# Kernel tuning notes

Hardware: AMD Instinct MI355X
Metric: run time of the kernel (lower is better)

The kernel has to match this reference:

```python
import jax, jax.numpy as jnp
import numpy as np

NEG = -1e4      # BigBird additive mask value
LN_EPS = 1e-12  # BERT-style LayerNorm eps


def _bigbird_forward(xs_pad, mask, Wq, bq, Wk, bk, Wv, bv, Wo, bo, gamma, beta, rand_idx):
    b, n, hsz = xs_pad.shape
    H = rand_idx.shape[0]
    nb = rand_idx.shape[1] + 2          # one rand row per non-edge query block
    BS = n // nb                        # block size
    d = hsz // H
    r = rand_idx.shape[2]
    scale = 1.0 / np.sqrt(d).astype(np.float32)

    mf = mask.reshape(b, n).astype(xs_pad.dtype)   # (b,n) 1=token, 0=pad
    mb = mf.reshape(b, nb, BS)                     # blocked mask

    def proj(W, bias):
        return (xs_pad @ W + bias).reshape(b, n, H, d).transpose(0, 2, 1, 3)

    q = proj(Wq, bq) * scale            # (b,H,n,d)
    k = proj(Wk, bk)
    v = proj(Wv, bv)
    qb = q.reshape(b, H, nb, BS, d)
    kb = k.reshape(b, H, nb, BS, d)
    vb = v.reshape(b, H, nb, BS, d)

    # ---- global rows: first / last query block attend to all keys ----
    def full_row(qi):                   # qi: (b,H,BS,d)
        s = jnp.einsum('bhqd,bhkd->bhqk', qi, k) + (1.0 - mf)[:, None, None, :] * NEG
        return jnp.einsum('bhqk,bhkd->bhqd', jax.nn.softmax(s, axis=-1), v)

    ctx_first = full_row(qb[:, :, 0])
    ctx_last = full_row(qb[:, :, nb - 1])

    # ---- random key/value blocks: per-head, per-query-block gather ----
    hidx = jnp.arange(H)[:, None, None]
    rand_k = kb[:, hidx, rand_idx].reshape(b, H, nb - 2, r * BS, d)
    rand_v = vb[:, hidx, rand_idx].reshape(b, H, nb - 2, r * BS, d)
    rand_m = mb[:, rand_idx].reshape(b, H, nb - 2, r * BS)

    def sparse_row(qi, kc, vc, mc):     # kc:(b,H,K,d), mc:(b,H,K)
        s = jnp.einsum('bhqd,bhkd->bhqk', qi, kc) + (1.0 - mc)[:, :, None, :] * NEG
        return jnp.einsum('bhqk,bhkd->bhqd', jax.nn.softmax(s, axis=-1), vc)

    def gather_blocks(ids, ridx):
        kc = jnp.concatenate([kb[:, :, j] for j in ids] + [rand_k[:, :, ridx]], axis=2)
        vc = jnp.concatenate([vb[:, :, j] for j in ids] + [rand_v[:, :, ridx]], axis=2)
        mc = jnp.concatenate([jnp.broadcast_to(mb[:, None, j], (b, H, BS)) for j in ids]
                             + [rand_m[:, :, ridx]], axis=2)
        return kc, vc, mc

    # second / penultimate query blocks: window + globals + rand
    ctx_second = sparse_row(qb[:, :, 1], *gather_blocks([0, 1, 2, nb - 1], 0))
    ctx_penult = sparse_row(qb[:, :, nb - 2], *gather_blocks([nb - 3, nb - 2, nb - 1, 0], nb - 3))

    # ---- middle rows i in [2, nb-3]: 3-block sliding window + first/last global + r random ----
    nmid = nb - 4
    mid = jnp.arange(2, nb - 2)
    win = mid[:, None] + jnp.arange(-1, 2)[None, :]        # (nmid,3)
    k_win = kb[:, :, win].reshape(b, H, nmid, 3 * BS, d)
    v_win = vb[:, :, win].reshape(b, H, nmid, 3 * BS, d)
    m_win = jnp.broadcast_to(mb[:, win].reshape(b, 1, nmid, 3 * BS), (b, H, nmid, 3 * BS))

    def rep_glob(t):                     # (b,H,BS,...) -> (b,H,nmid,BS,...)
        return jnp.broadcast_to(t[:, :, None], (b, H, nmid) + t.shape[2:])

    k_mid = jnp.concatenate([k_win, rep_glob(kb[:, :, 0]), rep_glob(kb[:, :, nb - 1]),
                             rand_k[:, :, 1:nb - 3]], axis=3)
    v_mid = jnp.concatenate([v_win, rep_glob(vb[:, :, 0]), rep_glob(vb[:, :, nb - 1]),
                             rand_v[:, :, 1:nb - 3]], axis=3)
    m_first = jnp.broadcast_to(mb[:, None, None, 0], (b, H, nmid, BS))
    m_last = jnp.broadcast_to(mb[:, None, None, nb - 1], (b, H, nmid, BS))
    m_mid = jnp.concatenate([m_win, m_first, m_last, rand_m[:, :, 1:nb - 3]], axis=3)

    s_mid = jnp.einsum('bhmqd,bhmkd->bhmqk', qb[:, :, 2:nb - 2], k_mid) \
            + (1.0 - m_mid)[:, :, :, None, :] * NEG
    ctx_mid = jnp.einsum('bhmqk,bhmkd->bhmqd', jax.nn.softmax(s_mid, axis=-1), v_mid)

    ctx = jnp.concatenate([ctx_first[:, :, None], ctx_second[:, :, None], ctx_mid,
                           ctx_penult[:, :, None], ctx_last[:, :, None]], axis=2)
    ctx = ctx.reshape(b, H, n, d).transpose(0, 2, 1, 3).reshape(b, n, hsz)
    ctx = ctx * mf[:, :, None]           # from_mask on output rows

    # BigBirdSelfOutput: dense + residual + LayerNorm (dropout=0 / eval)
    y = ctx @ Wo + bo + xs_pad
    mu = y.mean(-1, keepdims=True)
    var = ((y - mu) ** 2).mean(-1, keepdims=True)
    return (y - mu) * jax.lax.rsqrt(var + LN_EPS) * gamma + beta


def setup_inputs() -> dict:
    key = jax.random.key(0)
    ks = jax.random.split(key, 6)
    B, N, HSZ, H, BS, R = 4, 4096, 1024, 16, 64, 3
    NB = N // BS
    init = lambda k, shp: jax.random.normal(k, shp, dtype=jnp.float32) * 0.02
    return {
        'xs_pad': jax.random.normal(ks[0], (B, N, HSZ), dtype=jnp.float32),
        'mask': jnp.ones((B, 1, N), dtype=jnp.int32),
        'Wq': init(ks[1], (HSZ, HSZ)), 'bq': jnp.zeros((HSZ,), jnp.float32),
        'Wk': init(ks[2], (HSZ, HSZ)), 'bk': jnp.zeros((HSZ,), jnp.float32),
        'Wv': init(ks[3], (HSZ, HSZ)), 'bv': jnp.zeros((HSZ,), jnp.float32),
        'Wo': init(ks[4], (HSZ, HSZ)), 'bo': jnp.zeros((HSZ,), jnp.float32),
        'gamma': jnp.ones((HSZ,), jnp.float32), 'beta': jnp.zeros((HSZ,), jnp.float32),
        'rand_idx': jax.random.randint(ks[5], (H, NB - 2, R), 1, NB - 1).astype(jnp.int32),
    }


def reference(xs_pad, mask, Wq, bq, Wk, bk, Wv, bv, Wo, bo, gamma, beta, rand_idx):
    return _bigbird_forward(xs_pad, mask, Wq, bq, Wk, bk, Wv, bv, Wo, bo, gamma, beta, rand_idx)
```

## Files before the change

### kernel.cpp

```cpp
#include <hip/hip_runtime.h>
#include <hip/hip_bf16.h>

#define B_   4
#define N_   4096
#define HSZ  1024
#define H_   16
#define D_   64
#define NB_  64
#define R_   3
#define M_   (B_*N_)
#define NEGV (-1e4f)
#define LOG2E 1.4426950408889634f

typedef float f32x4 __attribute__((ext_vector_type(4)));
typedef short s16x8 __attribute__((ext_vector_type(8)));
typedef __bf16 b16x8 __attribute__((ext_vector_type(8)));

__device__ __forceinline__ f32x4 mfma16(s16x8 a, s16x8 b, f32x4 c) {
  return __builtin_amdgcn_mfma_f32_16x16x32_bf16(
      __builtin_bit_cast(b16x8, a), __builtin_bit_cast(b16x8, b), c, 0, 0, 0);
}

__device__ __forceinline__ short f2b(float x) {
  __hip_bfloat16 h = __float2bfloat16(x);
  return (short)__builtin_bit_cast(unsigned short, h);
}

__device__ __forceinline__ unsigned pack2(float a, float b) {
  return (unsigned)(unsigned short)f2b(a) |
         ((unsigned)(unsigned short)f2b(b) << 16);
}

__device__ __forceinline__ void gl_lds16(const short* g, short* l) {
  __builtin_amdgcn_global_load_lds(
      (const __attribute__((address_space(1))) unsigned int*)g,
      (__attribute__((address_space(3))) unsigned int*)l, 16, 0, 0);
}

__global__ __launch_bounds__(256) void k_conv(const float* __restrict__ in,
                                              short* __restrict__ out) {
  size_t i = ((size_t)blockIdx.x * 256 + threadIdx.x) * 8;
  float4 a = *(const float4*)&in[i];
  float4 b = *(const float4*)&in[i + 4];
  s16x8 o;
  o[0] = f2b(a.x); o[1] = f2b(a.y); o[2] = f2b(a.z); o[3] = f2b(a.w);
  o[4] = f2b(b.x); o[5] = f2b(b.y); o[6] = f2b(b.z); o[7] = f2b(b.w);
  *(s16x8*)&out[i] = o;
}

__global__ __launch_bounds__(256) void k_wt(const float* __restrict__ Wq,
                                            const float* __restrict__ Wk,
                                            const float* __restrict__ Wv,
                                            const float* __restrict__ Wo,
                                            short* __restrict__ out) {
  const int z = blockIdx.z;
  const float* src = (z == 0) ? Wq : (z == 1) ? Wk : (z == 2) ? Wv : Wo;
  short* dst = out + (size_t)z * HSZ * HSZ;
  __shared__ __align__(16) float t[64][68];
  const int tk = blockIdx.x * 64, tn = blockIdx.y * 64;
  const int tid = threadIdx.x;
#pragma unroll
  for (int r = 0; r < 4; ++r) {
    int c = tid + r * 256;
    int row = c >> 4, seg = c & 15;
    *(float4*)&t[row][seg * 4] =
        *(const float4*)&src[(size_t)(tk + row) * HSZ + tn + seg * 4];
  }
  __syncthreads();
#pragma unroll
  for (int r = 0; r < 2; ++r) {
    int c = tid + r * 256;
    int row = c >> 3, seg = c & 7;
    s16x8 o;
#pragma unroll
    for (int u = 0; u < 8; ++u) o[u] = f2b(t[seg * 8 + u][row]);
    *(s16x8*)&dst[(size_t)(tn + row) * HSZ + tk + seg * 8] = o;
  }
}

template <int PATH>
__global__ __launch_bounds__(256) void k_gemm(
    const short* __restrict__ A, const short* __restrict__ WT,
    const float* __restrict__ bias0, const float* __restrict__ bias1,
    short* __restrict__ o0, short* __restrict__ o1,
    const float* __restrict__ xs, float* __restrict__ yout) {
  const int z = (PATH == 0) ? blockIdx.z : 0;
  const int wsel = (PATH == 0) ? z : (PATH == 1 ? 2 : 3);
  const short* Bt = WT + (size_t)wsel * HSZ * HSZ;
  const float* bias = (PATH == 0 && z == 1) ? bias1 : bias0;
  short* outb = (PATH == 0 && z == 1) ? o1 : o0;
  const float alpha = (PATH == 0 && z == 0) ? 0.125f * LOG2E : 1.0f;

  __shared__ __align__(16) short a_lds[2][128][64];
  __shared__ __align__(16) short b_lds[2][128][64];

  const int tid = threadIdx.x, lane = tid & 63, wave = tid >> 6;
  const int lq = lane & 15, g = lane >> 4;
  const int wm = (wave & 1) * 64, wn = (wave >> 1) * 64;
  const int tm = blockIdx.x * 128, tn = blockIdx.y * 128;

  const int srow = wave * 32 + (lane >> 3);
  const int scol = ((lane & 7) ^ ((lane >> 3) & 7)) * 8;

  f32x4 acc[4][4] = {};

  auto STAGE = [&](int buf, int kt) {
#pragma unroll
    for (int u = 0; u < 4; ++u) {
      gl_lds16(&A[(size_t)(tm + srow + u * 8) * HSZ + kt + scol],
               &a_lds[buf][wave * 32 + u * 8][0]);
      gl_lds16(&Bt[(size_t)(tn + srow + u * 8) * HSZ + kt + scol],
               &b_lds[buf][wave * 32 + u * 8][0]);
    }
  };

  const int sw = (lq & 7) << 3;
  auto COMPUTE = [&](int buf) {
#pragma unroll
    for (int kk = 0; kk < 2; ++kk) {
      const int ko = (kk * 32 + g * 8) ^ sw;
      s16x8 af[4], bf[4];
#pragma unroll
      for (int i = 0; i < 4; ++i)
        af[i] = *(const s16x8*)&a_lds[buf][wm + i * 16 + lq][ko];
#pragma unroll
      for (int j = 0; j < 4; ++j)
        bf[j] = *(const s16x8*)&b_lds[buf][wn + j * 16 + lq][ko];
#pragma unroll
      for (int i = 0; i < 4; ++i)
#pragma unroll
        for (int j = 0; j < 4; ++j)
          acc[i][j] = (PATH == 1) ? mfma16(af[i], bf[j], acc[i][j])
                                  : mfma16(bf[j], af[i], acc[i][j]);
    }
  };

  STAGE(0, 0);
  STAGE(1, 64);
  int cur = 0;
  for (int s = 0; s < 14; ++s) {
    asm volatile("s_waitcnt vmcnt(8)" ::: "memory");
    __builtin_amdgcn_s_barrier();
    COMPUTE(cur);
    __builtin_amdgcn_s_barrier();
    STAGE(cur, (s + 2) * 64);
    cur ^= 1;
  }
  asm volatile("s_waitcnt vmcnt(8)" ::: "memory");
  __builtin_amdgcn_s_barrier();
  COMPUTE(cur);
  cur ^= 1;
  asm volatile("s_waitcnt vmcnt(0)" ::: "memory");
  __builtin_amdgcn_s_barrier();
  COMPUTE(cur);

  if (PATH == 1) {
#pragma unroll
    for (int j = 0; j < 4; ++j) {
      const int col = tn + wn + j * 16 + lq;
      const int hh = col >> 6, dd = col & 63;
      const float bi = bias[col];
#pragma unroll
      for (int i = 0; i < 4; ++i) {
        const int nrow = tm + wm + i * 16 + g * 4;
        const int bb = nrow >> 12, nn = nrow & (N_ - 1);
        uint2 w;
        w.x = pack2(acc[i][j][0] + bi, acc[i][j][1] + bi);
        w.y = pack2(acc[i][j][2] + bi, acc[i][j][3] + bi);
        *(uint2*)&o0[(((size_t)bb * H_ + hh) * D_ + dd) * N_ + nn] = w;
      }
    }
    return;
  }

#pragma unroll
  for (int i = 0; i < 4; ++i) {
    const int row = tm + wm + i * 16 + lq;
#pragma unroll
    for (int j = 0; j < 4; ++j) {
      const int colb = tn + wn + j * 16 + g * 4;
      const float4 bi = *(const float4*)&bias[colb];
      if (PATH == 0) {
        const int bb = row >> 12, nn = row & (N_ - 1);
        const int hh = colb >> 6, dd = colb & 63;
        uint2 w;
        w.x = pack2((acc[i][j][0] + bi.x) * alpha,
                    (acc[i][j][1] + bi.y) * alpha);
        w.y = pack2((acc[i][j][2] + bi.z) * alpha,
                    (acc[i][j][3] + bi.w) * alpha);
        *(uint2*)&outb[(((size_t)bb * H_ + hh) * N_ + nn) * D_ + dd] = w;
      } else {
        const size_t idx = (size_t)row * HSZ + colb;
        const float4 xv = *(const float4*)&xs[idx];
        float4 yv;
        yv.x = acc[i][j][0] + bi.x + xv.x;
        yv.y = acc[i][j][1] + bi.y + xv.y;
        yv.z = acc[i][j][2] + bi.z + xv.z;
        yv.w = acc[i][j][3] + bi.w + xv.w;
        *(float4*)&yout[idx] = yv;
      }
    }
  }
}

__global__ __launch_bounds__(256) void k_attn(
    const short* __restrict__ Q, const short* __restrict__ K,
    const short* __restrict__ VT, const int* __restrict__ mask,
    const int* __restrict__ rnd, short* __restrict__ ctx,
    float* __restrict__ pO, float* __restrict__ pm, float* __restrict__ pl) {
  const int orig = blockIdx.x;
  const int swg = (orig & 7) * 624 + (orig >> 3);
  const int s = swg % 78;
  const int bh_i = swg / 78;
  const int h = bh_i & 15, b = bh_i >> 4;
  const int tid = threadIdx.x, lane = tid & 63, wave = tid >> 6;
  const int g = lane >> 4, lq = lane & 15;

  __shared__ __align__(16) short k_lds[64][64];
  __shared__ __align__(16) short vt_lds[64][64];
  __shared__ __align__(16) short p_lds[4][16][72];
  __shared__ __align__(16) float bias_s[64];
  __shared__ int list_s[8];
  __shared__ int Ls;

  const bool mid = (s < 62);
  const int qb = mid ? (s + 1) : (((s - 62) >> 3) ? (NB_ - 1) : 0);

  if (tid == 0) {
    int L;
    if (!mid) {
      int chunk = (s - 62) & 7;
#pragma unroll
      for (int i = 0; i < 8; ++i) list_s[i] = chunk * 8 + i;
      L = 8;
    } else {
      const int* rp = rnd + ((size_t)h * (NB_ - 2) + (qb - 1)) * R_;
      int n;
      if (qb == 1) {
        list_s[0] = 0; list_s[1] = 1; list_s[2] = 2; list_s[3] = NB_ - 1; n = 4;
      } else if (qb == NB_ - 2) {
        list_s[0] = NB_ - 3; list_s[1] = NB_ - 2; list_s[2] = NB_ - 1;
        list_s[3] = 0; n = 4;
      } else {
        list_s[0] = qb - 1; list_s[1] = qb; list_s[2] = qb + 1;
        list_s[3] = 0; list_s[4] = NB_ - 1; n = 5;
      }
      for (int j = 0; j < R_; ++j) list_s[n + j] = rp[j];
      L = n + R_;
    }
    Ls = L;
  }

  const size_t bh = (size_t)b * H_ + h;
  const size_t qrow = bh * N_ + (size_t)qb * 64 + wave * 16 + lq;
  s16x8 qf0 = *(const s16x8*)&Q[qrow * D_ + g * 8];
  s16x8 qf1 = *(const s16x8*)&Q[qrow * D_ + 32 + g * 8];

  __syncthreads();
  const int L = Ls;

  const int r0 = tid >> 3, sg = tid & 7;
  const int csl = (sg ^ (r0 & 7)) * 8;
  const int sw = (lq & 7);

  const short* Kb = K + bh * (size_t)N_ * D_;
  const short* Vb = VT + bh * (size_t)D_ * N_;
  const int* mb = mask + (size_t)b * N_;

  s16x8 kr0, kr1, vr0, vr1;
  float br = 0.0f;
  {
    const int kb = list_s[0];
    const short* kp = Kb + (size_t)kb * 64 * D_;
    const short* vp = Vb + (size_t)kb * 64;
    kr0 = *(const s16x8*)&kp[(size_t)r0 * D_ + sg * 8];
    kr1 = *(const s16x8*)&kp[(size_t)(r0 + 32) * D_ + sg * 8];
    vr0 = *(const s16x8*)&vp[(size_t)r0 * N_ + sg * 8];
    vr1 = *(const s16x8*)&vp[(size_t)(r0 + 32) * N_ + sg * 8];
    if (tid < 64)
      br = (1.0f - (float)mb[kb * 64 + tid]) * (NEGV * LOG2E);
  }

  f32x4 o[4] = {};
  float m_run = -INFINITY, ssum = 0.0f;

  for (int it = 0; it < L; ++it) {
    *(s16x8*)&k_lds[r0][csl] = kr0;
    *(s16x8*)&k_lds[r0 + 32][csl] = kr1;
    *(s16x8*)&vt_lds[r0][csl] = vr0;
    *(s16x8*)&vt_lds[r0 + 32][csl] = vr1;
    if (tid < 64) bias_s[tid] = br;
    if (it + 1 < L) {
      const int kb = list_s[it + 1];
      const short* kp = Kb + (size_t)kb * 64 * D_;
      const short* vp = Vb + (size_t)kb * 64;
      kr0 = *(const s16x8*)&kp[(size_t)r0 * D_ + sg * 8];
      kr1 = *(const s16x8*)&kp[(size_t)(r0 + 32) * D_ + sg * 8];
      vr0 = *(const s16x8*)&vp[(size_t)r0 * N_ + sg * 8];
      vr1 = *(const s16x8*)&vp[(size_t)(r0 + 32) * N_ + sg * 8];
      if (tid < 64)
        br = (1.0f - (float)mb[kb * 64 + tid]) * (NEGV * LOG2E);
    }
    __syncthreads();

    f32x4 st[4];
#pragma unroll
    for (int f = 0; f < 4; ++f) {
      f32x4 a0 = {};
      s16x8 af0 = *(const s16x8*)&k_lds[f * 16 + lq][(g ^ sw) * 8];
      s16x8 af1 = *(const s16x8*)&k_lds[f * 16 + lq][((4 + g) ^ sw) * 8];
      a0 = mfma16(af0, qf0, a0);
      a0 = mfma16(af1, qf1, a0);
      st[f] = a0 + *(const f32x4*)&bias_s[f * 16 + g * 4];
    }

    float t0 = fmaxf(fmaxf(st[0][0], st[0][1]), fmaxf(st[0][2], st[0][3]));
    float t1 = fmaxf(fmaxf(st[1][0], st[1][1]), fmaxf(st[1][2], st[1][3]));
    float t2 = fmaxf(fmaxf(st[2][0], st[2][1]), fmaxf(st[2][2], st[2][3]));
    float t3 = fmaxf(fmaxf(st[3][0], st[3][1]), fmaxf(st[3][2], st[3][3]));
    float bm = fmaxf(fmaxf(t0, t1), fmaxf(t2, t3));
    bm = fmaxf(bm, __shfl_xor(bm, 16));
    bm = fmaxf(bm, __shfl_xor(bm, 32));
    if (!__all(bm <= m_run + 8.0f)) {
      float mnew = fmaxf(m_run, bm);
      float al = exp2f(m_run - mnew);
      f32x4 av;
      av[0] = __shfl(al, g * 4 + 0);
      av[1] = __shfl(al, g * 4 + 1);
      av[2] = __shfl(al, g * 4 + 2);
      av[3] = __shfl(al, g * 4 + 3);
#pragma unroll
      for (int j = 0; j < 4; ++j) o[j] *= av;
      ssum *= al;
      m_run = mnew;
    }
    float psum = 0.0f;
#pragma unroll
    for (int f = 0; f < 4; ++f)
#pragma unroll
      for (int e = 0; e < 4; ++e) {
        float pv = exp2f(st[f][e] - m_run);
        st[f][e] = pv;
        psum += pv;
      }
    psum += __shfl_xor(psum, 16);
    psum += __shfl_xor(psum, 32);
    ssum += psum;

#pragma unroll
    for (int f = 0; f < 4; ++f) {
      uint2 w = make_uint2(pack2(st[f][0], st[f][1]),
                           pack2(st[f][2], st[f][3]));
      *(uint2*)&p_lds[wave][lq][f * 16 + g * 4] = w;
    }

#pragma unroll
    for (int kk = 0; kk < 2; ++kk) {
      s16x8 pa = *(const s16x8*)&p_lds[wave][lq][kk * 32 + g * 8];
#pragma unroll
      for (int j = 0; j < 4; ++j) {
        s16x8 bv =
            *(const s16x8*)&vt_lds[j * 16 + lq][((kk * 4 + g) ^ sw) * 8];
        o[j] = mfma16(pa, bv, o[j]);
      }
    }
    __syncthreads();
  }

  if (mid) {
    float rs = (float)mb[qb * 64 + wave * 16 + lq] / ssum;
    float s0 = __shfl(rs, g * 4 + 0);
    float s1 = __shfl(rs, g * 4 + 1);
    float s2 = __shfl(rs, g * 4 + 2);
    float s3 = __shfl(rs, g * 4 + 3);
#pragma unroll
    for (int j = 0; j < 4; ++j) {
      k_lds[wave * 16 + g * 4 + 0][j * 16 + lq] = f2b(o[j][0] * s0);
      k_lds[wave * 16 + g * 4 + 1][j * 16 + lq] = f2b(o[j][1] * s1);
      k_lds[wave * 16 + g * 4 + 2][j * 16 + lq] = f2b(o[j][2] * s2);
      k_lds[wave * 16 + g * 4 + 3][j * 16 + lq] = f2b(o[j][3] * s3);
    }
    __syncthreads();
#pragma unroll
    for (int pp = 0; pp < 2; ++pp) {
      int c = tid + pp * 256;
      int row = c >> 3, seg = c & 7;
      *(s16x8*)&ctx[((size_t)b * N_ + qb * 64 + row) * HSZ + h * D_ + seg * 8] =
          *(const s16x8*)&k_lds[row][seg * 8];
    }
  } else {
    const int e2 = s - 62;
    const int qsel = e2 >> 3, chunk = e2 & 7;
    const size_t eidx = (bh * 2 + qsel) * 8 + chunk;
    float* po = pO + eidx * 4096;
#pragma unroll
    for (int j = 0; j < 4; ++j)
#pragma unroll
      for (int e = 0; e < 4; ++e)
        po[(wave * 16 + g * 4 + e) * 64 + j * 16 + lq] = o[j][e];
    if (lane < 16) {
      pm[eidx * 64 + wave * 16 + lane] = m_run;
      pl[eidx * 64 + wave * 16 + lane] = ssum;
    }
  }
}

__global__ __launch_bounds__(256) void k_comb(
    const float* __restrict__ pO, const float* __restrict__ pm,
    const float* __restrict__ pl, const int* __restrict__ mask,
    short* __restrict__ ctx) {
  const int qsel = blockIdx.x, h = blockIdx.y, b = blockIdx.z;
  const int qb = qsel ? NB_ - 1 : 0;
  const int tid = threadIdx.x;
  const int q = tid >> 2, dq = tid & 3;
  const size_t base = (((size_t)b * H_ + h) * 2 + qsel) * 8;

  float mv[8];
  float M = -INFINITY;
#pragma unroll
  for (int i = 0; i < 8; ++i) {
    mv[i] = pm[(base + i) * 64 + q];
    M = fmaxf(M, mv[i]);
  }
  float Lsum = 0.0f;
#pragma unroll
  for (int i = 0; i < 8; ++i) {
    float w = exp2f(mv[i] - M);
    mv[i] = w;
    Lsum += pl[(base + i) * 64 + q] * w;
  }
  f32x4 acc[4] = {};
#pragma unroll
  for (int i = 0; i < 8; ++i) {
    const float* p = pO + (base + i) * 4096 + q * 64 + dq * 16;
    float w = mv[i];
#pragma unroll
    for (int u = 0; u < 4; ++u) {
      f32x4 v = *(const f32x4*)&p[u * 4];
      acc[u] += v * w;
    }
  }
  float sc = (float)mask[(size_t)b * N_ + qb * 64 + q] / Lsum;
  s16x8 out0, out1;
#pragma unroll
  for (int u = 0; u < 8; ++u) {
    out0[u] = f2b(acc[u >> 2][u & 3] * sc);
    out1[u] = f2b(acc[2 + (u >> 2)][u & 3] * sc);
  }
  short* dst = &ctx[((size_t)b * N_ + qb * 64 + q) * HSZ + h * D_ + dq * 16];
  *(s16x8*)dst = out0;
  *(s16x8*)(dst + 8) = out1;
}

__global__ __launch_bounds__(256) void k_ln(float* __restrict__ y,
                                            const float* __restrict__ gamma,
                                            const float* __restrict__ beta) {
  const int row = blockIdx.x, tid = threadIdx.x, lane = tid & 63,
            wave = tid >> 6;
  __shared__ float s_sum[4], s_sq[4];
  float4 v = *(const float4*)&y[(size_t)row * HSZ + tid * 4];
  float s = v.x + v.y + v.z + v.w;
  float q = v.x * v.x + v.y * v.y + v.z * v.z + v.w * v.w;
#pragma unroll
  for (int m = 1; m <= 32; m <<= 1) {
    s += __shfl_xor(s, m);
    q += __shfl_xor(q, m);
  }
  if (lane == 0) { s_sum[wave] = s; s_sq[wave] = q; }
  __syncthreads();
  float S = s_sum[0] + s_sum[1] + s_sum[2] + s_sum[3];
  float Qs = s_sq[0] + s_sq[1] + s_sq[2] + s_sq[3];
  float mu = S * (1.0f / HSZ);
  float var = Qs * (1.0f / HSZ) - mu * mu;
  float r = rsqrtf(var + 1e-12f);
  float4 g = *(const float4*)&gamma[tid * 4];
  float4 be = *(const float4*)&beta[tid * 4];
  float4 outv;
  outv.x = (v.x - mu) * r * g.x + be.x;
  outv.y = (v.y - mu) * r * g.y + be.y;
  outv.z = (v.z - mu) * r * g.z + be.z;
  outv.w = (v.w - mu) * r * g.w + be.w;
  *(float4*)&y[(size_t)row * HSZ + tid * 4] = outv;
}

extern "C" void kernel_launch(void* const* d_in, const int* in_sizes, int n_in,
                              void* d_out, int out_size, void* d_ws,
                              size_t ws_size, hipStream_t stream) {
  const float* xs = (const float*)d_in[0];
  const int* mask = (const int*)d_in[1];
  const float* Wq = (const float*)d_in[2];
  const float* bq = (const float*)d_in[3];
  const float* Wk = (const float*)d_in[4];
  const float* bk = (const float*)d_in[5];
  const float* Wv = (const float*)d_in[6];
  const float* bv = (const float*)d_in[7];
  const float* Wo = (const float*)d_in[8];
  const float* bo = (const float*)d_in[9];
  const float* gamma = (const float*)d_in[10];
  const float* beta = (const float*)d_in[11];
  const int* rnd = (const int*)d_in[12];
  float* yout = (float*)d_out;

  char* ws = (char*)d_ws;
  const size_t SZ_XS = (size_t)M_ * HSZ * 2;
  const size_t SZ_WT = (size_t)4 * HSZ * HSZ * 2;
  short* xsb = (short*)ws;
  short* wt = (short*)(ws + SZ_XS);
  short* qbuf = (short*)(ws + SZ_XS + SZ_WT);
  short* kbuf = qbuf + (size_t)M_ * HSZ;
  short* vtb = kbuf + (size_t)M_ * HSZ;
  char* after = ws + SZ_XS + SZ_WT + 3 * SZ_XS;
  float* pO = (float*)(after + (1 << 20));
  float* pm = pO + (size_t)1024 * 4096;
  float* pl = pm + (size_t)1024 * 64;

  k_conv<<<8192, 256, 0, stream>>>(xs, xsb);
  k_wt<<<dim3(16, 16, 4), 256, 0, stream>>>(Wq, Wk, Wv, Wo, wt);
  k_gemm<0><<<dim3(128, 8, 2), 256, 0, stream>>>(
      xsb, wt, bq, bk, qbuf, kbuf, nullptr, nullptr);
  k_gemm<1><<<dim3(128, 8, 1), 256, 0, stream>>>(
      xsb, wt, bv, nullptr, vtb, nullptr, nullptr, nullptr);
  k_attn<<<4992, 256, 0, stream>>>(qbuf, kbuf, vtb, mask, rnd, xsb, pO, pm,
                                   pl);
  k_comb<<<dim3(2, H_, B_), 256, 0, stream>>>(pO, pm, pl, mask, xsb);
  k_gemm<2><<<dim3(128, 8, 1), 256, 0, stream>>>(
      xsb, wt, bo, nullptr, nullptr, nullptr, xs, yout);
  k_ln<<<M_, 256, 0, stream>>>(yout, gamma, beta);
}
```

Baseline: 357.2 us.

## Drop online-softmax max tracking and remap GEMM block order

The attention kernel no longer computes a per-block row max and rescales conditionally. It exponentiates scores directly, relative to a coarse shift, and renormalises by 2^-24 only when any running sum exceeds 2^24. This removes the max reductions and shuffles from each key-block iteration. The cost is a risk of overflow or underflow if score magnitudes are large: there is no guard against a single exp2 overflowing. Separately, the GEMM launches switch to a 1D grid with a swizzled tile mapping, meant to improve L2 reuse of the weight tiles.

```diff
diff --git a/kernel.cpp b/kernel.cpp
--- a/kernel.cpp
+++ b/kernel.cpp
@@ -97,7 +97,9 @@
   const int tid = threadIdx.x, lane = tid & 63, wave = tid >> 6;
   const int lq = lane & 15, g = lane >> 4;
   const int wm = (wave & 1) * 64, wn = (wave >> 1) * 64;
-  const int tm = blockIdx.x * 128, tn = blockIdx.y * 128;
+  const int orig = blockIdx.x;
+  const int swg = (orig & 7) * 128 + (orig >> 3);
+  const int tm = (swg >> 3) * 128, tn = (swg & 7) * 128;
 
   const int srow = wave * 32 + (lane >> 3);
   const int scol = ((lane & 7) ^ ((lane >> 3) & 7)) * 8;
@@ -282,7 +284,7 @@
   }
 
   f32x4 o[4] = {};
-  float m_run = -INFINITY, ssum = 0.0f;
+  float mshift = 0.0f, ssum = 0.0f;
 
   for (int it = 0; it < L; ++it) {
     *(s16x8*)&k_lds[r0][csl] = kr0;
@@ -306,43 +308,34 @@
     f32x4 st[4];
 #pragma unroll
     for (int f = 0; f < 4; ++f) {
-      f32x4 a0 = {};
+      f32x4 a0 = *(const f32x4*)&bias_s[f * 16 + g * 4];
       s16x8 af0 = *(const s16x8*)&k_lds[f * 16 + lq][(g ^ sw) * 8];
       s16x8 af1 = *(const s16x8*)&k_lds[f * 16 + lq][((4 + g) ^ sw) * 8];
       a0 = mfma16(af0, qf0, a0);
       a0 = mfma16(af1, qf1, a0);
-      st[f] = a0 + *(const f32x4*)&bias_s[f * 16 + g * 4];
-    }
-
-    float t0 = fmaxf(fmaxf(st[0][0], st[0][1]), fmaxf(st[0][2], st[0][3]));
-    float t1 = fmaxf(fmaxf(st[1][0], st[1][1]), fmaxf(st[1][2], st[1][3]));
-    float t2 = fmaxf(fmaxf(st[2][0], st[2][1]), fmaxf(st[2][2], st[2][3]));
-    float t3 = fmaxf(fmaxf(st[3][0], st[3][1]), fmaxf(st[3][2], st[3][3]));
-    float bm = fmaxf(fmaxf(t0, t1), fmaxf(t2, t3));
-    bm = fmaxf(bm, __shfl_xor(bm, 16));
-    bm = fmaxf(bm, __shfl_xor(bm, 32));
-    if (!__all(bm <= m_run + 8.0f)) {
-      float mnew = fmaxf(m_run, bm);
-      float al = exp2f(m_run - mnew);
-      f32x4 av;
-      av[0] = __shfl(al, g * 4 + 0);
-      av[1] = __shfl(al, g * 4 + 1);
-      av[2] = __shfl(al, g * 4 + 2);
-      av[3] = __shfl(al, g * 4 + 3);
-#pragma unroll
-      for (int j = 0; j < 4; ++j) o[j] *= av;
-      ssum *= al;
-      m_run = mnew;
-    }
+      st[f] = a0;
+    }
+
     float psum = 0.0f;
-#pragma unroll
-    for (int f = 0; f < 4; ++f)
-#pragma unroll
-      for (int e = 0; e < 4; ++e) {
-        float pv = exp2f(st[f][e] - m_run);
-        st[f][e] = pv;
-        psum += pv;
-      }
+    if (mshift == 0.0f) {
+#pragma unroll
+      for (int f = 0; f < 4; ++f)
+#pragma unroll
+        for (int e = 0; e < 4; ++e) {
+          float pv = exp2f(st[f][e]);
+          st[f][e] = pv;
+          psum += pv;
+        }
+    } else {
+#pragma unroll
+      for (int f = 0; f < 4; ++f)
+#pragma unroll
+        for (int e = 0; e < 4; ++e) {
+          float pv = exp2f(st[f][e] - mshift);
+          st[f][e] = pv;
+          psum += pv;
+        }
+    }
     psum += __shfl_xor(psum, 16);
     psum += __shfl_xor(psum, 32);
     ssum += psum;
@@ -364,11 +357,18 @@
         o[j] = mfma16(pa, bv, o[j]);
       }
     }
+
+    if (__any(ssum > 16777216.0f)) {
+#pragma unroll
+      for (int j = 0; j < 4; ++j) o[j] *= 5.9604645e-08f;
+      ssum *= 5.9604645e-08f;
+      mshift += 24.0f;
+    }
     __syncthreads();
   }
 
   if (mid) {
-    float rs = (float)mb[qb * 64 + wave * 16 + lq] / ssum;
+    float rs = (float)mb[qb * 64 + wave * 16 + lq] / fmaxf(ssum, 1e-30f);
     float s0 = __shfl(rs, g * 4 + 0);
     float s1 = __shfl(rs, g * 4 + 1);
     float s2 = __shfl(rs, g * 4 + 2);
@@ -399,7 +399,7 @@
       for (int e = 0; e < 4; ++e)
         po[(wave * 16 + g * 4 + e) * 64 + j * 16 + lq] = o[j][e];
     if (lane < 16) {
-      pm[eidx * 64 + wave * 16 + lane] = m_run;
+      pm[eidx * 64 + wave * 16 + lane] = mshift;
       pl[eidx * 64 + wave * 16 + lane] = ssum;
     }
   }
@@ -440,7 +440,7 @@
       acc[u] += v * w;
     }
   }
-  float sc = (float)mask[(size_t)b * N_ + qb * 64 + q] / Lsum;
+  float sc = (float)mask[(size_t)b * N_ + qb * 64 + q] / fmaxf(Lsum, 1e-30f);
   s16x8 out0, out1;
 #pragma unroll
   for (int u = 0; u < 8; ++u) {
@@ -516,14 +516,14 @@
 
   k_conv<<<8192, 256, 0, stream>>>(xs, xsb);
   k_wt<<<dim3(16, 16, 4), 256, 0, stream>>>(Wq, Wk, Wv, Wo, wt);
-  k_gemm<0><<<dim3(128, 8, 2), 256, 0, stream>>>(
+  k_gemm<0><<<dim3(1024, 1, 2), 256, 0, stream>>>(
       xsb, wt, bq, bk, qbuf, kbuf, nullptr, nullptr);
-  k_gemm<1><<<dim3(128, 8, 1), 256, 0, stream>>>(
+  k_gemm<1><<<dim3(1024, 1, 1), 256, 0, stream>>>(
       xsb, wt, bv, nullptr, vtb, nullptr, nullptr, nullptr);
   k_attn<<<4992, 256, 0, stream>>>(qbuf, kbuf, vtb, mask, rnd, xsb, pO, pm,
                                    pl);
   k_comb<<<dim3(2, H_, B_), 256, 0, stream>>>(pO, pm, pl, mask, xsb);
-  k_gemm<2><<<dim3(128, 8, 1), 256, 0, stream>>>(
+  k_gemm<2><<<dim3(1024, 1, 1), 256, 0, stream>>>(
       xsb, wt, bo, nullptr, nullptr, nullptr, xs, yout);
   k_ln<<<M_, 256, 0, stream>>>(yout, gamma, beta);
 }
```

After: 336.8 us. 1.06x faster.
